# Performance work log

Hardware: AMD Instinct MI355X
Metric: run time of the kernel (lower is better)

## Reference

```python
import jax, jax.numpy as jnp
import numpy as np

DEGREE = 8


def setup_inputs() -> dict:
    key = jax.random.key(0)
    k1, k2 = jax.random.split(key)
    b, c_in, c_out = 16384, 512, 512
    x = jax.random.normal(k1, (b, c_in), dtype=jnp.float32)
    std = 1.0 / (c_in * (DEGREE + 1))
    cheby_coeffs = jax.random.normal(k2, (c_in, c_out, DEGREE + 1), dtype=jnp.float32) * std
    return {"x": x, "cheby_coeffs": cheby_coeffs}


def reference(x, cheby_coeffs):
    # x: (b, c_in); cheby_coeffs: (c_in, c_out, degree+1)
    arange = jnp.arange(DEGREE + 1, dtype=x.dtype)  # (d+1,)
    # double tanh squashes into (-1, 1), then Chebyshev basis via acos/cos
    t = jnp.arccos(jnp.tanh(jnp.tanh(x)))            # (b, c_in)
    basis = jnp.cos(t[:, :, None] * arange)          # (b, c_in, d+1)
    y = jnp.einsum('bid,iod->bo', basis, cheby_coeffs)
    return y
```

## Files before the change

### kernel.cpp

```cpp
#include <hip/hip_runtime.h>
#include <hip/hip_bf16.h>
#include <stdint.h>

#define CIN   512
#define COUT  512
#define BM    128
#define BN    256
#define NIB   16
#define KSTEPS 128

typedef float f32x4 __attribute__((ext_vector_type(4)));
typedef short s16x8 __attribute__((ext_vector_type(8)));

__device__ uint4 Wp_g[KSTEPS * 32 * 64];
__device__ float bias_g[COUT];

__device__ __forceinline__ uint32_t cvtpk(float lo, float hi) {
  uint32_t r;
  asm("v_cvt_pk_bf16_f32 %0, %1, %2" : "=v"(r) : "v"(lo), "v"(hi));
  return r;
}

__device__ __forceinline__ float ftanh(float v) {
  float e = __expf(v + v);
  return 1.0f - __fdividef(2.0f, e + 1.0f);
}

__global__ void pack_w(const float* __restrict__ cw) {
  __shared__ float lf[32 * 144];
  int ib = blockIdx.x >> 5;
  int cg = blockIdx.x & 31;
  for (int r = threadIdx.x; r < 32 * 144; r += 256) {
    int il = r / 144;
    int rem = r - il * 144;
    lf[r] = cw[(size_t)(ib * 32 + il) * (COUT * 9) + cg * 144 + rem];
  }
  __syncthreads();
  for (int v = threadIdx.x; v < 512; v += 256) {
    int ksl = v >> 6;
    int lane = v & 63;
    int d = ksl + 1;
    int lh = lane >> 4, l15 = lane & 15;
    uint32_t p[4];
    #pragma unroll
    for (int q = 0; q < 4; ++q) {
      float a = lf[(lh * 8 + 2 * q    ) * 144 + l15 * 9 + d];
      float b = lf[(lh * 8 + 2 * q + 1) * 144 + l15 * 9 + d];
      p[q] = cvtpk(a, b);
    }
    Wp_g[((ib * 8 + ksl) * 32 + cg) * 64 + lane] = make_uint4(p[0], p[1], p[2], p[3]);
  }
}

__global__ void bias_k(const float* __restrict__ cw) {
  int o = blockIdx.x;
  int t = threadIdx.x;
  float s = 0.f;
  #pragma unroll
  for (int q = 0; q < 8; ++q)
    s += cw[(size_t)(t + 64 * q) * (COUT * 9) + o * 9];
  #pragma unroll
  for (int off = 32; off; off >>= 1) s += __shfl_down(s, off);
  if (t == 0) bias_g[o] = s;
}

__global__ void __launch_bounds__(512, 1) cheby_gemm(const float* __restrict__ x,
                                                     float* __restrict__ out) {
  __shared__ uint4 lds[2 * 4 * 4 * BM];
  const int tid  = threadIdx.x;
  const int lane = tid & 63;
  const int l15  = lane & 15;
  const int lh   = lane >> 4;
  const int w    = tid >> 6;
  const int wr   = w >> 2;
  const int wc   = w & 3;

  int b0  = blockIdx.x;
  int bid = (b0 & 7) * 32 + (b0 >> 3);
  const int rb  = (bid >> 1) * BM;
  const int cb  = bid & 1;
  const int ocb = cb * BN;
  const int cgbase = cb * 16 + wc * 4;

  const int ge   = w >> 1;
  const int grow = (w & 1) * 64 + lane;
  const float* xrow = x + (size_t)(rb + grow) * CIN + ge * 8;

  const uint4* pB = Wp_g + (size_t)cgbase * 64 + lane;

  f32x4 acc[4][4];
  #pragma unroll
  for (int cf = 0; cf < 4; ++cf) {
    float bv = bias_g[ocb + wc * 64 + cf * 16 + l15];
    #pragma unroll
    for (int rf = 0; rf < 4; ++rf) {
      acc[rf][cf][0] = bv; acc[rf][cf][1] = bv;
      acc[rf][cf][2] = bv; acc[rf][cf][3] = bv;
    }
  }

  float xv[8], u2[8], tm1[8], tm2[8];

  auto loadX = [&](int ib) {
    const float4* p = reinterpret_cast<const float4*>(xrow + ib * 32);
    float4 v0 = p[0], v1 = p[1];
    xv[0] = v0.x; xv[1] = v0.y; xv[2] = v0.z; xv[3] = v0.w;
    xv[4] = v1.x; xv[5] = v1.y; xv[6] = v1.z; xv[7] = v1.w;
  };
  auto compute_u = [&]() {
    #pragma unroll
    for (int k = 0; k < 8; ++k) {
      float u = ftanh(ftanh(xv[k]));
      tm1[k] = u; tm2[k] = 1.0f; u2[k] = u + u;
    }
  };
  auto advance = [&]() {
    #pragma unroll
    for (int k = 0; k < 8; ++k) {
      float t = __builtin_fmaf(u2[k], tm1[k], -tm2[k]);
      tm2[k] = tm1[k]; tm1[k] = t;
    }
  };
  auto emit = [&](int buf, int slot) {
    uint32_t p0 = cvtpk(tm1[0], tm1[1]);
    uint32_t p1 = cvtpk(tm1[2], tm1[3]);
    uint32_t p2 = cvtpk(tm1[4], tm1[5]);
    uint32_t p3 = cvtpk(tm1[6], tm1[7]);
    lds[((buf * 4 + slot) * 4 + ge) * BM + grow] = make_uint4(p0, p1, p2, p3);
  };

  s16x8 aA[4], aB[4];
  s16x8 breg[2][4];
  auto loadB = [&](int par, int ks) {
    #pragma unroll
    for (int cf = 0; cf < 4; ++cf) {
      uint4 v = pB[(size_t)ks * 2048 + cf * 64];
      breg[par][cf] = __builtin_bit_cast(s16x8, v);
    }
  };
  auto dsreadA = [&](s16x8 (&dst)[4], int buf, int slot) {
    int base = ((buf * 4 + slot) * 4 + lh) * BM + wr * 64 + l15;
    #pragma unroll
    for (int rf = 0; rf < 4; ++rf)
      dst[rf] = *reinterpret_cast<const s16x8*>(&lds[base + rf * 16]);
  };
  auto barrier_pre = [&]() {
    asm volatile("s_waitcnt lgkmcnt(0)" ::: "memory");
    __builtin_amdgcn_sched_barrier(0);
    __builtin_amdgcn_s_barrier();
  };
  auto mfma16 = [&](s16x8 (&a)[4], int par) {
    __builtin_amdgcn_s_setprio(1);
    #pragma unroll
    for (int rf = 0; rf < 4; ++rf) {
      #pragma unroll
      for (int cf = 0; cf < 4; ++cf)
        acc[rf][cf] = __builtin_amdgcn_mfma_f32_16x16x32_bf16(
            a[rf], breg[par][cf], acc[rf][cf], 0, 0, 0);
    }
    __builtin_amdgcn_s_setprio(0);
    __builtin_amdgcn_s_barrier();
  };

  loadX(0);
  compute_u();
  emit(0, 0);
  advance(); emit(0, 1);
  advance(); emit(0, 2);
  advance(); emit(0, 3);
  loadB(0, 0);
  barrier_pre();
  dsreadA(aA, 0, 0);

  for (int ib = 0; ib < NIB; ++ib) {
    if (ib + 1 < NIB) loadX(ib + 1);

    #pragma unroll
    for (int j = 0; j < 4; ++j) {
      int ks = ib * 8 + j;
      if (j < 3) { if (j & 1) dsreadA(aA, 0, j + 1); else dsreadA(aB, 0, j + 1); }
      else       dsreadA(aA, 1, 0);
      loadB((j + 1) & 1, ks + 1);
      advance(); emit(1, j);
      barrier_pre();
      if (j & 1) mfma16(aB, 1); else mfma16(aA, 0);
    }

    #pragma unroll
    for (int j = 0; j < 4; ++j) {
      int ks = ib * 8 + 4 + j;
      if (j < 3) { if (j & 1) dsreadA(aA, 1, j + 1); else dsreadA(aB, 1, j + 1); }
      else if (ib + 1 < NIB) dsreadA(aA, 0, 0);
      if (ks + 1 < KSTEPS) loadB((j + 1) & 1, ks + 1);
      if (ib + 1 < NIB) {
        if (j == 0) { compute_u(); emit(0, 0); }
        else        { advance();   emit(0, j); }
      }
      barrier_pre();
      if (j & 1) mfma16(aB, 1); else mfma16(aA, 0);
    }
  }

  const int orow = rb + wr * 64 + lh * 4;
  const int ocol = ocb + wc * 64 + l15;
  #pragma unroll
  for (int rf = 0; rf < 4; ++rf) {
    #pragma unroll
    for (int cf = 0; cf < 4; ++cf) {
      #pragma unroll
      for (int r = 0; r < 4; ++r)
        out[(size_t)(orow + rf * 16 + r) * COUT + ocol + cf * 16] = acc[rf][cf][r];
    }
  }
}

extern "C" void kernel_launch(void* const* d_in, const int* in_sizes, int n_in,
                              void* d_out, int out_size, void* d_ws, size_t ws_size,
                              hipStream_t stream) {
  const float* x  = (const float*)d_in[0];
  const float* cw = (const float*)d_in[1];
  float* out = (float*)d_out;

  pack_w<<<dim3(512), dim3(256), 0, stream>>>(cw);
  bias_k<<<dim3(COUT), dim3(64), 0, stream>>>(cw);
  cheby_gemm<<<dim3(256), dim3(512), 0, stream>>>(x, out);
}
```

Baseline: 101.2 us.

## Shrink GEMM tile to 128x128 with 4 waves and per-half barriers

Halves the output tile width, so each block now runs 4 waves (256 threads) with two blocks per CU and twice as many blocks in the grid. Each wave computes 16 Chebyshev inputs instead of 8. Synchronisation moves from one barrier per k-step to one barrier per half-buffer of four k-steps, and the LDS reads for A now happen inline right before the MFMAs rather than being prefetched a step ahead. The goal is less barrier overhead and better latency hiding through two resident blocks per CU. In exchange, each block computes the basis for only half as many output columns, so the basis work per output doubles, and register pressure from the wider per-thread arrays rises.

```diff
diff --git a/kernel.cpp b/kernel.cpp
--- a/kernel.cpp
+++ b/kernel.cpp
@@ -5,7 +5,7 @@
 #define CIN   512
 #define COUT  512
 #define BM    128
-#define BN    256
+#define BN    128
 #define NIB   16
 #define KSTEPS 128
 
@@ -24,6 +24,12 @@
 __device__ __forceinline__ float ftanh(float v) {
   float e = __expf(v + v);
   return 1.0f - __fdividef(2.0f, e + 1.0f);
+}
+
+__device__ __forceinline__ void lds_barrier() {
+  asm volatile("s_waitcnt lgkmcnt(0)" ::: "memory");
+  __builtin_amdgcn_s_barrier();
+  asm volatile("" ::: "memory");
 }
 
 __global__ void pack_w(const float* __restrict__ cw) {
@@ -64,7 +70,7 @@
   if (t == 0) bias_g[o] = s;
 }
 
-__global__ void __launch_bounds__(512, 1) cheby_gemm(const float* __restrict__ x,
+__global__ void __launch_bounds__(256, 2) cheby_gemm(const float* __restrict__ x,
                                                      float* __restrict__ out) {
   __shared__ uint4 lds[2 * 4 * 4 * BM];
   const int tid  = threadIdx.x;
@@ -72,19 +78,19 @@
   const int l15  = lane & 15;
   const int lh   = lane >> 4;
   const int w    = tid >> 6;
-  const int wr   = w >> 2;
-  const int wc   = w & 3;
+  const int wr   = w >> 1;
+  const int wc   = w & 1;
 
   int b0  = blockIdx.x;
-  int bid = (b0 & 7) * 32 + (b0 >> 3);
-  const int rb  = (bid >> 1) * BM;
-  const int cb  = bid & 1;
+  int bid = (b0 & 7) * 64 + (b0 >> 3);
+  const int rb  = (bid >> 2) * BM;
+  const int cb  = bid & 3;
   const int ocb = cb * BN;
-  const int cgbase = cb * 16 + wc * 4;
-
-  const int ge   = w >> 1;
-  const int grow = (w & 1) * 64 + lane;
-  const float* xrow = x + (size_t)(rb + grow) * CIN + ge * 8;
+  const int cgbase = cb * 8 + wc * 4;
+
+  const int c0   = wr * 2;
+  const int grow = wc * 64 + lane;
+  const float* xrow = x + (size_t)(rb + grow) * CIN + c0 * 8;
 
   const uint4* pB = Wp_g + (size_t)cgbase * 64 + lane;
 
@@ -99,37 +105,40 @@
     }
   }
 
-  float xv[8], u2[8], tm1[8], tm2[8];
+  float xv[16], u2[16], tm1[16], tm2[16];
 
   auto loadX = [&](int ib) {
     const float4* p = reinterpret_cast<const float4*>(xrow + ib * 32);
-    float4 v0 = p[0], v1 = p[1];
-    xv[0] = v0.x; xv[1] = v0.y; xv[2] = v0.z; xv[3] = v0.w;
-    xv[4] = v1.x; xv[5] = v1.y; xv[6] = v1.z; xv[7] = v1.w;
+    #pragma unroll
+    for (int q = 0; q < 4; ++q) {
+      float4 v = p[q];
+      xv[4*q+0] = v.x; xv[4*q+1] = v.y; xv[4*q+2] = v.z; xv[4*q+3] = v.w;
+    }
   };
   auto compute_u = [&]() {
     #pragma unroll
-    for (int k = 0; k < 8; ++k) {
+    for (int k = 0; k < 16; ++k) {
       float u = ftanh(ftanh(xv[k]));
       tm1[k] = u; tm2[k] = 1.0f; u2[k] = u + u;
     }
   };
   auto advance = [&]() {
     #pragma unroll
-    for (int k = 0; k < 8; ++k) {
+    for (int k = 0; k < 16; ++k) {
       float t = __builtin_fmaf(u2[k], tm1[k], -tm2[k]);
       tm2[k] = tm1[k]; tm1[k] = t;
     }
   };
   auto emit = [&](int buf, int slot) {
-    uint32_t p0 = cvtpk(tm1[0], tm1[1]);
-    uint32_t p1 = cvtpk(tm1[2], tm1[3]);
-    uint32_t p2 = cvtpk(tm1[4], tm1[5]);
-    uint32_t p3 = cvtpk(tm1[6], tm1[7]);
-    lds[((buf * 4 + slot) * 4 + ge) * BM + grow] = make_uint4(p0, p1, p2, p3);
-  };
-
-  s16x8 aA[4], aB[4];
+    uint32_t q0 = cvtpk(tm1[0],  tm1[1]),  q1 = cvtpk(tm1[2],  tm1[3]);
+    uint32_t q2 = cvtpk(tm1[4],  tm1[5]),  q3 = cvtpk(tm1[6],  tm1[7]);
+    uint32_t q4 = cvtpk(tm1[8],  tm1[9]),  q5 = cvtpk(tm1[10], tm1[11]);
+    uint32_t q6 = cvtpk(tm1[12], tm1[13]), q7 = cvtpk(tm1[14], tm1[15]);
+    int base = (buf * 4 + slot) * 4;
+    lds[(base + c0    ) * BM + grow] = make_uint4(q0, q1, q2, q3);
+    lds[(base + c0 + 1) * BM + grow] = make_uint4(q4, q5, q6, q7);
+  };
+
   s16x8 breg[2][4];
   auto loadB = [&](int par, int ks) {
     #pragma unroll
@@ -138,18 +147,12 @@
       breg[par][cf] = __builtin_bit_cast(s16x8, v);
     }
   };
-  auto dsreadA = [&](s16x8 (&dst)[4], int buf, int slot) {
+  auto mfma_step = [&](int buf, int slot, int par) {
+    s16x8 a[4];
     int base = ((buf * 4 + slot) * 4 + lh) * BM + wr * 64 + l15;
     #pragma unroll
     for (int rf = 0; rf < 4; ++rf)
-      dst[rf] = *reinterpret_cast<const s16x8*>(&lds[base + rf * 16]);
-  };
-  auto barrier_pre = [&]() {
-    asm volatile("s_waitcnt lgkmcnt(0)" ::: "memory");
-    __builtin_amdgcn_sched_barrier(0);
-    __builtin_amdgcn_s_barrier();
-  };
-  auto mfma16 = [&](s16x8 (&a)[4], int par) {
+      a[rf] = *reinterpret_cast<const s16x8*>(&lds[base + rf * 16]);
     __builtin_amdgcn_s_setprio(1);
     #pragma unroll
     for (int rf = 0; rf < 4; ++rf) {
@@ -159,7 +162,6 @@
             a[rf], breg[par][cf], acc[rf][cf], 0, 0, 0);
     }
     __builtin_amdgcn_s_setprio(0);
-    __builtin_amdgcn_s_barrier();
   };
 
   loadX(0);
@@ -169,8 +171,7 @@
   advance(); emit(0, 2);
   advance(); emit(0, 3);
   loadB(0, 0);
-  barrier_pre();
-  dsreadA(aA, 0, 0);
+  lds_barrier();
 
   for (int ib = 0; ib < NIB; ++ib) {
     if (ib + 1 < NIB) loadX(ib + 1);
@@ -178,27 +179,23 @@
     #pragma unroll
     for (int j = 0; j < 4; ++j) {
       int ks = ib * 8 + j;
-      if (j < 3) { if (j & 1) dsreadA(aA, 0, j + 1); else dsreadA(aB, 0, j + 1); }
-      else       dsreadA(aA, 1, 0);
       loadB((j + 1) & 1, ks + 1);
+      mfma_step(0, j, j & 1);
       advance(); emit(1, j);
-      barrier_pre();
-      if (j & 1) mfma16(aB, 1); else mfma16(aA, 0);
-    }
+    }
+    lds_barrier();
 
     #pragma unroll
     for (int j = 0; j < 4; ++j) {
       int ks = ib * 8 + 4 + j;
-      if (j < 3) { if (j & 1) dsreadA(aA, 1, j + 1); else dsreadA(aB, 1, j + 1); }
-      else if (ib + 1 < NIB) dsreadA(aA, 0, 0);
       if (ks + 1 < KSTEPS) loadB((j + 1) & 1, ks + 1);
+      mfma_step(1, j, j & 1);
       if (ib + 1 < NIB) {
         if (j == 0) { compute_u(); emit(0, 0); }
         else        { advance();   emit(0, j); }
       }
-      barrier_pre();
-      if (j & 1) mfma16(aB, 1); else mfma16(aA, 0);
-    }
+    }
+    lds_barrier();
   }
 
   const int orow = rb + wr * 64 + lh * 4;
@@ -223,5 +220,5 @@
 
   pack_w<<<dim3(512), dim3(256), 0, stream>>>(cw);
   bias_k<<<dim3(COUT), dim3(64), 0, stream>>>(cw);
-  cheby_gemm<<<dim3(256), dim3(512), 0, stream>>>(x, out);
-}
+  cheby_gemm<<<dim3(512), dim3(256), 0, stream>>>(x, out);
+}
```

New measurement: 112.9 us. 11.6% more time.
